# Performance work log

Measured on AMD Instinct MI355X. Metric: run time of the kernel, lower is better.

The kernel has to match this reference:

```python
import jax, jax.numpy as jnp
import numpy as np

N = 50000       # nodes
E = 800000      # edges
D_IN = 128      # input_dim
HID = 256       # hidden_dim
HEADS = 4
FH = HID // 4   # per-head out dim = 64
OUT = 8         # output_dim
NEG_SLOPE = 0.2 # GATConv leaky_relu slope


def setup_inputs() -> dict:
    key = jax.random.key(0)
    ks = jax.random.split(key, 16)
    def glorot(k, shape):
        fan_in, fan_out = shape[0], shape[-1]
        s = jnp.sqrt(6.0 / (fan_in + fan_out))
        return jax.random.uniform(k, shape, jnp.float32, -s, s)
    inp = {
        "x": jax.random.normal(ks[0], (N, D_IN), jnp.float32),
        "edge_index": jax.random.randint(ks[1], (2, E), 0, N, jnp.int64),
        # GCN layers
        "W1": glorot(ks[2], (D_IN, HID)), "b1": jnp.zeros((HID,), jnp.float32),
        "W2": glorot(ks[3], (HID, HID)), "b2": jnp.zeros((HID,), jnp.float32),
        "W3": glorot(ks[4], (HID, HID // 2)), "b3": jnp.zeros((HID // 2,), jnp.float32),
        # GAT layer: in = HID//2 = 128, out per head = FH, 4 heads concat -> HID
        "Wg": glorot(ks[5], (HID // 2, HEADS * FH)),
        "a_src": glorot(ks[6], (HEADS, FH)),
        "a_dst": glorot(ks[7], (HEADS, FH)),
        "bg": jnp.zeros((HEADS * FH,), jnp.float32),
        # classifier MLP: HID -> HID//2 -> HID//4 -> OUT
        "Wc1": glorot(ks[8], (HID, HID // 2)), "bc1": jnp.zeros((HID // 2,), jnp.float32),
        "Wc2": glorot(ks[9], (HID // 2, HID // 4)), "bc2": jnp.zeros((HID // 4,), jnp.float32),
        "Wc3": glorot(ks[10], (HID // 4, OUT)), "bc3": jnp.zeros((OUT,), jnp.float32),
    }
    return inp


def _with_self_loops(edge_index, n):
    loop = jnp.arange(n, dtype=edge_index.dtype)
    src = jnp.concatenate([edge_index[0], loop])
    dst = jnp.concatenate([edge_index[1], loop])
    return src, dst


def gcn_conv(x, W, b, src, dst, n):
    # PyG GCNConv: h = X W; out = D^{-1/2}(A+I)D^{-1/2} h + b (self loops in src/dst)
    h = x @ W
    deg = jax.ops.segment_sum(jnp.ones_like(dst, jnp.float32), dst, num_segments=n)
    dinv = jnp.where(deg > 0, jax.lax.rsqrt(deg), 0.0)
    norm = dinv[src] * dinv[dst]                      # [E+N]
    out = jax.ops.segment_sum(h[src] * norm[:, None], dst, num_segments=n)
    return out + b


def gat_conv(x, Wg, a_src, a_dst, bg, src, dst, n):
    # PyG GATConv (eval mode, no attn dropout), self loops included in src/dst
    h = (x @ Wg).reshape(n, HEADS, FH)                # [N,H,F]
    al_s = jnp.einsum('nhf,hf->nh', h, a_src)         # [N,H]
    al_d = jnp.einsum('nhf,hf->nh', h, a_dst)
    e = jax.nn.leaky_relu(al_s[src] + al_d[dst], NEG_SLOPE)  # [E+N,H]
    m = jax.ops.segment_max(e, dst, num_segments=n)   # per-dst stable softmax
    ex = jnp.exp(e - m[dst])
    den = jax.ops.segment_sum(ex, dst, num_segments=n)
    alpha = ex / den[dst]                             # [E+N,H]
    out = jax.ops.segment_sum(h[src] * alpha[:, :, None], dst, num_segments=n)
    return out.reshape(n, HEADS * FH) + bg


def reference(x, edge_index, W1, b1, W2, b2, W3, b3, Wg, a_src, a_dst, bg,
              Wc1, bc1, Wc2, bc2, Wc3, bc3):
    n = x.shape[0]
    src, dst = _with_self_loops(edge_index, n)
    h1 = jax.nn.relu(gcn_conv(x, W1, b1, src, dst, n))
    h2 = jax.nn.relu(gcn_conv(h1, W2, b2, src, dst, n)) + h1
    h3 = jax.nn.relu(gcn_conv(h2, W3, b3, src, dst, n))
    h_att = jax.nn.relu(gat_conv(h3, Wg, a_src, a_dst, bg, src, dst, n))
    h_pooled = jnp.mean(h_att, axis=0, keepdims=True)           # [1, HID]
    z = jax.nn.relu(h_pooled @ Wc1 + bc1)
    z = jax.nn.relu(z @ Wc2 + bc2)
    return z @ Wc3 + bc3                                        # [1, OUT]
```

## Files before the change

kernel.cpp:

```cpp
#include <hip/hip_runtime.h>
#include <hip/hip_bf16.h>

#define NNODES 50000
#define NEDGES 800000
#define EN 850000
#define SCAN_B 196

typedef __attribute__((ext_vector_type(8))) short bf16x8;
typedef __attribute__((ext_vector_type(4))) float f32x4;

__device__ __forceinline__ float bf2f(unsigned short u) {
    return __uint_as_float(((unsigned)u) << 16);
}
__device__ __forceinline__ float bflo(unsigned u) { return __uint_as_float(u << 16); }
__device__ __forceinline__ float bfhi(unsigned u) { return __uint_as_float(u & 0xffff0000u); }
__device__ __forceinline__ unsigned short f2bf(float x) {
    unsigned u = __float_as_uint(x);
    u += 0x7fffu + ((u >> 16) & 1u);
    return (unsigned short)(u >> 16);
}
__device__ __forceinline__ unsigned pack2bf(float a, float b) {
    return (unsigned)f2bf(a) | ((unsigned)f2bf(b) << 16);
}
__device__ __forceinline__ void acc8(float* acc, uint4 v, float wg) {
    acc[0] += bflo(v.x) * wg; acc[1] += bfhi(v.x) * wg;
    acc[2] += bflo(v.y) * wg; acc[3] += bfhi(v.y) * wg;
    acc[4] += bflo(v.z) * wg; acc[5] += bfhi(v.z) * wg;
    acc[6] += bflo(v.w) * wg; acc[7] += bfhi(v.w) * wg;
}

__device__ __forceinline__ void split_bf(float x, unsigned short& h, unsigned short& l) {
    unsigned u = __float_as_uint(x);
    h = (unsigned short)(u >> 16);
    float r = x - __uint_as_float(u & 0xffff0000u);
    l = (unsigned short)(__float_as_uint(r) >> 16);
}
__device__ __forceinline__ void do_split(const float* W, unsigned short* Wh, unsigned short* Wl,
                                         int i, int K, int N) {
    int n = i / K, k = i - n * K;
    unsigned short h, l;
    split_bf(W[(size_t)k * N + n], h, l);
    Wh[i] = h; Wl[i] = l;
}

__global__ __launch_bounds__(256) void prep_kernel(const int* __restrict__ ei, float* __restrict__ deg,
                                                   const float* __restrict__ x, unsigned short* __restrict__ xbf,
                                                   const float* __restrict__ W1, const float* __restrict__ W2,
                                                   const float* __restrict__ W3, const float* __restrict__ Wg,
                                                   unsigned short* __restrict__ W1th, unsigned short* __restrict__ W1tl,
                                                   unsigned short* __restrict__ W2th, unsigned short* __restrict__ W2tl,
                                                   unsigned short* __restrict__ W3th, unsigned short* __restrict__ W3tl,
                                                   unsigned short* __restrict__ Wgth, unsigned short* __restrict__ Wgtl) {
    int idx = blockIdx.x * 256 + threadIdx.x;
    atomicAdd(&deg[ei[NEDGES + idx]], 1.0f);
    {
        float4 a = *(const float4*)&x[(size_t)idx * 8];
        float4 b = *(const float4*)&x[(size_t)idx * 8 + 4];
        uint4 o;
        o.x = pack2bf(a.x, a.y); o.y = pack2bf(a.z, a.w);
        o.z = pack2bf(b.x, b.y); o.w = pack2bf(b.z, b.w);
        *(uint4*)&xbf[(size_t)idx * 8] = o;
    }
    if (idx < 32768)        do_split(W1, W1th, W1tl, idx, 128, 256);
    else if (idx < 98304)   do_split(W2, W2th, W2tl, idx - 32768, 256, 256);
    else if (idx < 131072)  do_split(W3, W3th, W3tl, idx - 98304, 256, 128);
    else if (idx < 163840)  do_split(Wg, Wgth, Wgtl, idx - 131072, 128, 256);
}

__global__ __launch_bounds__(256) void scan_part1(const float* __restrict__ deg, int* __restrict__ row,
                                                  int* __restrict__ bsum, float* __restrict__ dinv) {
    __shared__ int sdata[256];
    int t = threadIdx.x;
    int idx = blockIdx.x * 256 + t;
    float dg = idx < NNODES ? deg[idx] : 0.f;
    if (idx < NNODES) dinv[idx] = rsqrtf(dg + 1.0f);
    int v = idx < NNODES ? (int)dg + 1 : 0;
    sdata[t] = v;
    __syncthreads();
    for (int off = 1; off < 256; off <<= 1) {
        int tmp = t >= off ? sdata[t - off] : 0;
        __syncthreads();
        sdata[t] += tmp;
        __syncthreads();
    }
    if (idx < NNODES) row[idx] = sdata[t] - v;
    if (t == 255) bsum[blockIdx.x] = sdata[255];
}

__global__ __launch_bounds__(256) void scan_part2(int* __restrict__ bsum, int* __restrict__ bofs,
                                                  int* __restrict__ row) {
    __shared__ int sdata[256];
    int t = threadIdx.x;
    int v = t < SCAN_B ? bsum[t] : 0;
    sdata[t] = v;
    __syncthreads();
    for (int off = 1; off < 256; off <<= 1) {
        int tmp = t >= off ? sdata[t - off] : 0;
        __syncthreads();
        sdata[t] += tmp;
        __syncthreads();
    }
    if (t < SCAN_B) bofs[t] = sdata[t] - v;
    if (t == 0) row[NNODES] = EN;
}

__global__ __launch_bounds__(256) void scan_part3(int* __restrict__ row, const int* __restrict__ bofs) {
    int idx = blockIdx.x * 256 + threadIdx.x;
    if (idx < NNODES) row[idx] += bofs[blockIdx.x];
}

__global__ __launch_bounds__(256) void scatter_kernel(const int* __restrict__ ei, const int* __restrict__ row,
                                                      int* __restrict__ cursor, const float* __restrict__ dinv,
                                                      uint2* __restrict__ csr) {
    int e = blockIdx.x * blockDim.x + threadIdx.x;
    if (e >= EN) return;
    int s, d;
    if (e < NEDGES) { s = ei[e]; d = ei[NEDGES + e]; } else { s = e - NEDGES; d = s; }
    int pos = row[d] + atomicAdd(&cursor[d], 1);
    csr[pos] = make_uint2((unsigned)s, __float_as_uint(dinv[s] * dinv[d]));
}

template<int MODE>
__global__ __launch_bounds__(256) void gemm_bf(const unsigned short* __restrict__ A,
                                               const unsigned short* __restrict__ Wth,
                                               const unsigned short* __restrict__ Wtl,
                                               const float* __restrict__ bias,
                                               const float* __restrict__ asr, const float* __restrict__ ads,
                                               float* __restrict__ als, float* __restrict__ ald,
                                               unsigned short* __restrict__ C, int M, int K, int Nc) {
    __shared__ unsigned short As[128][40];
    __shared__ unsigned short Bh[128][40], Bl[128][40];
    int t = threadIdx.x;
    int row0 = blockIdx.x * 128, col0 = blockIdx.y * 128;
    int lane = t & 63, w = t >> 6;
    int mb = (w >> 1) * 64, nb = (w & 1) * 64;
    int lr = lane & 15, kg = (lane >> 4) * 8;

    f32x4 acc[4][4];
#pragma unroll
    for (int i = 0; i < 4; ++i)
#pragma unroll
        for (int j = 0; j < 4; ++j) acc[i][j] = (f32x4){0.f, 0.f, 0.f, 0.f};

    for (int k0 = 0; k0 < K; k0 += 32) {
#pragma unroll
        for (int it = 0; it < 2; ++it) {
            int q = it * 256 + t;
            int row = q >> 2, seg = (q & 3) * 8;
            int grow = row0 + row;
            uint4 v = make_uint4(0, 0, 0, 0);
            if (grow < M) v = *(const uint4*)&A[(size_t)grow * K + k0 + seg];
            *(uint4*)&As[row][seg] = v;
        }
#pragma unroll
        for (int it = 0; it < 2; ++it) {
            int o = it * 256 + t;
            int n = o >> 2, ko = (o & 3) * 8;
            size_t g = (size_t)(col0 + n) * K + k0 + ko;
            *(uint4*)&Bh[n][ko] = *(const uint4*)&Wth[g];
            *(uint4*)&Bl[n][ko] = *(const uint4*)&Wtl[g];
        }
        __syncthreads();

        bf16x8 a[4], bh[4], bl[4];
#pragma unroll
        for (int mf = 0; mf < 4; ++mf) a[mf] = *(const bf16x8*)&As[mb + mf * 16 + lr][kg];
#pragma unroll
        for (int nf = 0; nf < 4; ++nf) {
            bh[nf] = *(const bf16x8*)&Bh[nb + nf * 16 + lr][kg];
            bl[nf] = *(const bf16x8*)&Bl[nb + nf * 16 + lr][kg];
        }
#pragma unroll
        for (int mf = 0; mf < 4; ++mf)
#pragma unroll
            for (int nf = 0; nf < 4; ++nf) {
                acc[mf][nf] = __builtin_amdgcn_mfma_f32_16x16x32_bf16(a[mf], bh[nf], acc[mf][nf], 0, 0, 0);
                acc[mf][nf] = __builtin_amdgcn_mfma_f32_16x16x32_bf16(a[mf], bl[nf], acc[mf][nf], 0, 0, 0);
            }
        __syncthreads();
    }

    float s1[16], s2[16];
    if (MODE == 2) {
#pragma unroll
        for (int q = 0; q < 16; ++q) { s1[q] = 0.f; s2[q] = 0.f; }
    }

#pragma unroll
    for (int nf = 0; nf < 4; ++nf) {
        int col = col0 + nb + nf * 16 + lr;
        float bv = (MODE == 1) ? bias[col] : 0.f;
        float av = 0.f, dv = 0.f;
        if (MODE == 2) { av = asr[col]; dv = ads[col]; }
#pragma unroll
        for (int mf = 0; mf < 4; ++mf) {
#pragma unroll
            for (int r = 0; r < 4; ++r) {
                int row = row0 + mb + mf * 16 + (lane >> 4) * 4 + r;
                if (row < M) {
                    float v = acc[mf][nf][r];
                    if (MODE == 1) v = fmaxf(v + bv, 0.f);
                    C[(size_t)row * Nc + col] = f2bf(v);
                    if (MODE == 2) {
                        s1[mf * 4 + r] += v * av;
                        s2[mf * 4 + r] += v * dv;
                    }
                }
            }
        }
    }
    if (MODE == 2) {
        int head = (col0 + nb) >> 6;
#pragma unroll
        for (int q = 0; q < 16; ++q) {
#pragma unroll
            for (int off = 1; off < 16; off <<= 1) {
                s1[q] += __shfl_xor(s1[q], off);
                s2[q] += __shfl_xor(s2[q], off);
            }
        }
        if (lr == 0) {
#pragma unroll
            for (int mf = 0; mf < 4; ++mf) {
#pragma unroll
                for (int r = 0; r < 4; ++r) {
                    int row = row0 + mb + mf * 16 + (lane >> 4) * 4 + r;
                    if (row < M) {
                        als[row * 4 + head] = s1[mf * 4 + r];
                        ald[row * 4 + head] = s2[mf * 4 + r];
                    }
                }
            }
        }
    }
}

template<int NC, int MODE>
__global__ __launch_bounds__(256) void gcn_agg_bf(const unsigned short* __restrict__ h, const int* __restrict__ row,
                                                  const uint2* __restrict__ csr,
                                                  const float* __restrict__ b, const unsigned short* __restrict__ res,
                                                  unsigned short* __restrict__ out) {
    int wid = (int)((blockIdx.x * blockDim.x + threadIdx.x) >> 6);
    if (wid >= NNODES) return;
    int lane = threadIdx.x & 63;
    constexpr int LPE = NC / 8;
    constexpr int EPI = 64 / LPE;
    int sub = lane / LPE, li = lane % LPE;
    int col = li * 8;
    float acc[8];
#pragma unroll
    for (int i = 0; i < 8; ++i) acc[i] = 0.f;
    int j0 = row[wid], j1 = row[wid + 1];
    int j = j0 + sub;
    for (; j + 3 * EPI < j1; j += 4 * EPI) {
        uint2 c0 = csr[j], c1 = csr[j + EPI], c2 = csr[j + 2 * EPI], c3 = csr[j + 3 * EPI];
        uint4 v0 = *(const uint4*)&h[(size_t)c0.x * NC + col];
        uint4 v1 = *(const uint4*)&h[(size_t)c1.x * NC + col];
        uint4 v2 = *(const uint4*)&h[(size_t)c2.x * NC + col];
        uint4 v3 = *(const uint4*)&h[(size_t)c3.x * NC + col];
        acc8(acc, v0, __uint_as_float(c0.y));
        acc8(acc, v1, __uint_as_float(c1.y));
        acc8(acc, v2, __uint_as_float(c2.y));
        acc8(acc, v3, __uint_as_float(c3.y));
    }
    for (; j < j1; j += EPI) {
        uint2 c0 = csr[j];
        uint4 v0 = *(const uint4*)&h[(size_t)c0.x * NC + col];
        acc8(acc, v0, __uint_as_float(c0.y));
    }
#pragma unroll
    for (int i = 0; i < 8; ++i) {
        acc[i] += __shfl_xor(acc[i], 32);
        if constexpr (EPI == 4) acc[i] += __shfl_xor(acc[i], 16);
    }
    if (lane < LPE) {
        if constexpr (MODE >= 1) {
#pragma unroll
            for (int i = 0; i < 8; ++i) acc[i] = fmaxf(acc[i] + b[col + i], 0.f);
        }
        if constexpr (MODE == 2) {
            uint4 rv = *(const uint4*)&res[(size_t)wid * NC + col];
            acc8(acc, rv, 1.0f);
        }
        uint4 o;
        o.x = pack2bf(acc[0], acc[1]); o.y = pack2bf(acc[2], acc[3]);
        o.z = pack2bf(acc[4], acc[5]); o.w = pack2bf(acc[6], acc[7]);
        *(uint4*)&out[(size_t)wid * NC + col] = o;
    }
}

__device__ __forceinline__ float lrelu(float x) { return x < 0.f ? 0.2f * x : x; }

__global__ __launch_bounds__(256) void gat_csr(const unsigned short* __restrict__ hg, const int* __restrict__ row,
                                               const uint2* __restrict__ csr, const float* __restrict__ als,
                                               const float* __restrict__ ald, const float* __restrict__ bg,
                                               unsigned short* __restrict__ out) {
    __shared__ float alds[4][64][4];
    int wid = (int)((blockIdx.x * blockDim.x + threadIdx.x) >> 6);
    if (wid >= NNODES) return;
    int wv = threadIdx.x >> 6;
    int lane = threadIdx.x & 63;
    int j0 = row[wid], j1 = row[wid + 1];
    int deg = j1 - j0;
    float4 ad = *(const float4*)&ald[wid * 4];
    int sub = lane >> 5, li = lane & 31;
    int h = li >> 3;
    int col = li * 8;
    float acc[8];
#pragma unroll
    for (int i = 0; i < 8; ++i) acc[i] = 0.f;

    if (deg <= 64) {
        int sreg = 0;
        float e0 = -1e30f, e1 = -1e30f, e2 = -1e30f, e3 = -1e30f;
        if (lane < deg) {
            sreg = (int)csr[j0 + lane].x;
            float4 as4 = *(const float4*)&als[sreg * 4];
            e0 = lrelu(as4.x + ad.x); e1 = lrelu(as4.y + ad.y);
            e2 = lrelu(as4.z + ad.z); e3 = lrelu(as4.w + ad.w);
        }
        float m0 = e0, m1 = e1, m2 = e2, m3 = e3;
#pragma unroll
        for (int off = 32; off >= 1; off >>= 1) {
            m0 = fmaxf(m0, __shfl_xor(m0, off));
            m1 = fmaxf(m1, __shfl_xor(m1, off));
            m2 = fmaxf(m2, __shfl_xor(m2, off));
            m3 = fmaxf(m3, __shfl_xor(m3, off));
        }
        float x0 = __expf(e0 - m0), x1 = __expf(e1 - m1);
        float x2 = __expf(e2 - m2), x3 = __expf(e3 - m3);
        float d0 = x0, d1 = x1, d2 = x2, d3 = x3;
#pragma unroll
        for (int off = 32; off >= 1; off >>= 1) {
            d0 += __shfl_xor(d0, off);
            d1 += __shfl_xor(d1, off);
            d2 += __shfl_xor(d2, off);
            d3 += __shfl_xor(d3, off);
        }
        float i0 = 1.f / d0, i1 = 1.f / d1, i2 = 1.f / d2, i3 = 1.f / d3;
        *(float4*)&alds[wv][lane][0] = make_float4(x0 * i0, x1 * i1, x2 * i2, x3 * i3);
        int k = sub;
        for (; k + 6 < deg; k += 8) {
            int s0 = __shfl(sreg, k),     s1 = __shfl(sreg, k + 2);
            int s2 = __shfl(sreg, k + 4), s3 = __shfl(sreg, k + 6);
            float a0 = alds[wv][k][h],     a1 = alds[wv][k + 2][h];
            float a2 = alds[wv][k + 4][h], a3 = alds[wv][k + 6][h];
            uint4 v0 = *(const uint4*)&hg[(size_t)s0 * 256 + col];
            uint4 v1 = *(const uint4*)&hg[(size_t)s1 * 256 + col];
            uint4 v2 = *(const uint4*)&hg[(size_t)s2 * 256 + col];
            uint4 v3 = *(const uint4*)&hg[(size_t)s3 * 256 + col];
            acc8(acc, v0, a0); acc8(acc, v1, a1);
            acc8(acc, v2, a2); acc8(acc, v3, a3);
        }
        for (; k < deg; k += 2) {
            int s0 = __shfl(sreg, k);
            float a0 = alds[wv][k][h];
            uint4 v0 = *(const uint4*)&hg[(size_t)s0 * 256 + col];
            acc8(acc, v0, a0);
        }
    } else {
        float m0 = -1e30f, m1 = -1e30f, m2 = -1e30f, m3 = -1e30f;
        float d0 = 0.f, d1 = 0.f, d2 = 0.f, d3 = 0.f;
        for (int j = j0 + lane; j < j1; j += 64) {
            int s = (int)csr[j].x;
            float4 as4 = *(const float4*)&als[s * 4];
            m0 = fmaxf(m0, lrelu(as4.x + ad.x));
            m1 = fmaxf(m1, lrelu(as4.y + ad.y));
            m2 = fmaxf(m2, lrelu(as4.z + ad.z));
            m3 = fmaxf(m3, lrelu(as4.w + ad.w));
        }
#pragma unroll
        for (int off = 32; off >= 1; off >>= 1) {
            m0 = fmaxf(m0, __shfl_xor(m0, off));
            m1 = fmaxf(m1, __shfl_xor(m1, off));
            m2 = fmaxf(m2, __shfl_xor(m2, off));
            m3 = fmaxf(m3, __shfl_xor(m3, off));
        }
        for (int j = j0 + lane; j < j1; j += 64) {
            int s = (int)csr[j].x;
            float4 as4 = *(const float4*)&als[s * 4];
            d0 += __expf(lrelu(as4.x + ad.x) - m0);
            d1 += __expf(lrelu(as4.y + ad.y) - m1);
            d2 += __expf(lrelu(as4.z + ad.z) - m2);
            d3 += __expf(lrelu(as4.w + ad.w) - m3);
        }
#pragma unroll
        for (int off = 32; off >= 1; off >>= 1) {
            d0 += __shfl_xor(d0, off);
            d1 += __shfl_xor(d1, off);
            d2 += __shfl_xor(d2, off);
            d3 += __shfl_xor(d3, off);
        }
        float mh   = h == 0 ? m0 : h == 1 ? m1 : h == 2 ? m2 : m3;
        float invh = 1.f / (h == 0 ? d0 : h == 1 ? d1 : h == 2 ? d2 : d3);
        float adh  = h == 0 ? ad.x : h == 1 ? ad.y : h == 2 ? ad.z : ad.w;
        for (int j = j0 + sub; j < j1; j += 2) {
            uint2 c0 = csr[j];
            float a0 = __expf(lrelu(als[c0.x * 4 + h] + adh) - mh) * invh;
            uint4 v0 = *(const uint4*)&hg[(size_t)c0.x * 256 + col];
            acc8(acc, v0, a0);
        }
    }

#pragma unroll
    for (int i = 0; i < 8; ++i) acc[i] += __shfl_xor(acc[i], 32);
    if (lane < 32) {
        uint4 o;
        o.x = pack2bf(fmaxf(acc[0] + bg[col], 0.f),     fmaxf(acc[1] + bg[col + 1], 0.f));
        o.y = pack2bf(fmaxf(acc[2] + bg[col + 2], 0.f), fmaxf(acc[3] + bg[col + 3], 0.f));
        o.z = pack2bf(fmaxf(acc[4] + bg[col + 4], 0.f), fmaxf(acc[5] + bg[col + 5], 0.f));
        o.w = pack2bf(fmaxf(acc[6] + bg[col + 6], 0.f), fmaxf(acc[7] + bg[col + 7], 0.f));
        *(uint4*)&out[(size_t)wid * 256 + col] = o;
    }
}

__global__ __launch_bounds__(256) void pool_kernel(const unsigned short* __restrict__ hatt, float* __restrict__ ppart) {
    int col = threadIdx.x;
    int r0 = blockIdx.x * 256;
    int r1 = r0 + 256 < NNODES ? r0 + 256 : NNODES;
    float s = 0.f;
    for (int r = r0; r < r1; ++r) s += bf2f(hatt[(size_t)r * 256 + col]);
    ppart[blockIdx.x * 256 + col] = s;
}

__global__ __launch_bounds__(256) void mlp_kernel(const float* __restrict__ ppart,
                                                  const float* __restrict__ Wc1, const float* __restrict__ bc1,
                                                  const float* __restrict__ Wc2, const float* __restrict__ bc2,
                                                  const float* __restrict__ Wc3, const float* __restrict__ bc3,
                                                  float* __restrict__ out) {
    __shared__ float p[256], z1[128], z2[64];
    int t = threadIdx.x;
    float s0 = 0.f;
    for (int b = 0; b < SCAN_B; ++b) s0 += ppart[b * 256 + t];
    p[t] = s0 * (1.0f / NNODES);
    __syncthreads();
    if (t < 128) {
        float s = bc1[t];
        for (int k = 0; k < 256; ++k) s += p[k] * Wc1[k * 128 + t];
        z1[t] = fmaxf(s, 0.f);
    }
    __syncthreads();
    if (t < 64) {
        float s = bc2[t];
        for (int k = 0; k < 128; ++k) s += z1[k] * Wc2[k * 64 + t];
        z2[t] = fmaxf(s, 0.f);
    }
    __syncthreads();
    if (t < 8) {
        float s = bc3[t];
        for (int k = 0; k < 64; ++k) s += z2[k] * Wc3[k * 8 + t];
        out[t] = s;
    }
}

extern "C" void kernel_launch(void* const* d_in, const int* in_sizes, int n_in,
                              void* d_out, int out_size, void* d_ws, size_t ws_size,
                              hipStream_t stream) {
    const float* x   = (const float*)d_in[0];
    const int*   ei  = (const int*)d_in[1];
    const float* W1  = (const float*)d_in[2];  const float* b1  = (const float*)d_in[3];
    const float* W2  = (const float*)d_in[4];  const float* b2  = (const float*)d_in[5];
    const float* W3  = (const float*)d_in[6];  const float* b3  = (const float*)d_in[7];
    const float* Wg  = (const float*)d_in[8];
    const float* asr = (const float*)d_in[9];  const float* ads = (const float*)d_in[10];
    const float* bg  = (const float*)d_in[11];
    const float* Wc1 = (const float*)d_in[12]; const float* bc1 = (const float*)d_in[13];
    const float* Wc2 = (const float*)d_in[14]; const float* bc2 = (const float*)d_in[15];
    const float* Wc3 = (const float*)d_in[16]; const float* bc3 = (const float*)d_in[17];
    float* out = (float*)d_out;

    char* w = (char*)d_ws;
    float* deg    = (float*)w; w += (size_t)NNODES * 4;
    int*   cursor = (int*)w;   w += (size_t)NNODES * 4;
    float* dinv   = (float*)w; w += (size_t)NNODES * 4;
    int*   rowp   = (int*)w;   w += 200016;
    int*   bsum   = (int*)w;   w += 256 * 4;
    int*   bofs   = (int*)w;   w += 256 * 4;
    uint2* csr    = (uint2*)w; w += (size_t)EN * 8;
    float* als    = (float*)w; w += (size_t)NNODES * 4 * 4;
    float* ald    = (float*)w; w += (size_t)NNODES * 4 * 4;
    float* ppart  = (float*)w; w += (size_t)SCAN_B * 256 * 4;
    unsigned short* W1th = (unsigned short*)w; w += 128 * 256 * 2;
    unsigned short* W1tl = (unsigned short*)w; w += 128 * 256 * 2;
    unsigned short* W2th = (unsigned short*)w; w += 256 * 256 * 2;
    unsigned short* W2tl = (unsigned short*)w; w += 256 * 256 * 2;
    unsigned short* W3th = (unsigned short*)w; w += 256 * 128 * 2;
    unsigned short* W3tl = (unsigned short*)w; w += 256 * 128 * 2;
    unsigned short* Wgth = (unsigned short*)w; w += 128 * 256 * 2;
    unsigned short* Wgtl = (unsigned short*)w; w += 128 * 256 * 2;
    unsigned short* U1 = (unsigned short*)w; w += (size_t)NNODES * 256 * 2;
    unsigned short* U2 = (unsigned short*)w; w += (size_t)NNODES * 256 * 2;
    unsigned short* U3 = (unsigned short*)w; w += (size_t)NNODES * 256 * 2;
    unsigned short* U4 = (unsigned short*)w; w += (size_t)NNODES * 256 * 2;

    hipMemsetAsync(deg, 0, (size_t)NNODES * 8, stream);
    prep_kernel<<<3125, 256, 0, stream>>>(ei, deg, x, U1, W1, W2, W3, Wg,
                                          W1th, W1tl, W2th, W2tl, W3th, W3tl, Wgth, Wgtl);
    scan_part1<<<SCAN_B, 256, 0, stream>>>(deg, rowp, bsum, dinv);
    scan_part2<<<1, 256, 0, stream>>>(bsum, bofs, rowp);
    scan_part3<<<SCAN_B, 256, 0, stream>>>(rowp, bofs);
    scatter_kernel<<<(EN + 255) / 256, 256, 0, stream>>>(ei, rowp, cursor, dinv, csr);

    dim3 gA((NNODES + 127) / 128, 2);
    dim3 gB((NNODES + 127) / 128, 1);
    int aggBlocks = (NNODES * 64 + 255) / 256;

    gcn_agg_bf<128, 0><<<aggBlocks, 256, 0, stream>>>(U1, rowp, csr, nullptr, nullptr, U2);
    gemm_bf<1><<<gA, 256, 0, stream>>>(U2, W1th, W1tl, b1, nullptr, nullptr, nullptr, nullptr, U3, NNODES, 128, 256);

    gemm_bf<0><<<gA, 256, 0, stream>>>(U3, W2th, W2tl, nullptr, nullptr, nullptr, nullptr, nullptr, U1, NNODES, 256, 256);
    gcn_agg_bf<256, 2><<<aggBlocks, 256, 0, stream>>>(U1, rowp, csr, b2, U3, U2);

    gemm_bf<0><<<gB, 256, 0, stream>>>(U2, W3th, W3tl, nullptr, nullptr, nullptr, nullptr, nullptr, U4, NNODES, 256, 128);
    gcn_agg_bf<128, 1><<<aggBlocks, 256, 0, stream>>>(U4, rowp, csr, b3, nullptr, U1);

    gemm_bf<2><<<gA, 256, 0, stream>>>(U1, Wgth, Wgtl, nullptr, asr, ads, als, ald, U2, NNODES, 128, 256);
    gat_csr<<<aggBlocks, 256, 0, stream>>>(U2, rowp, csr, als, ald, bg, U3);

    pool_kernel<<<SCAN_B, 256, 0, stream>>>(U3, ppart);
    mlp_kernel<<<1, 256, 0, stream>>>(ppart, Wc1, bc1, Wc2, bc2, Wc3, bc3, out);
}
```

Baseline: 533.2 us.

## Fold attention logits into agg epilogue, fuse pooling into GAT, drop scan pass

Precomputes Wg·a_src and Wg·a_dst in the prep kernel so the per-node attention logits come from the third GCN aggregation epilogue, not from the GAT GEMM epilogue. The GAT kernel now writes per-block pooled partial sums instead of the full bf16 attention output, and a new reduce kernel feeds the MLP. The third scan pass is removed by adding the block offset wherever row pointers are read. This cuts one full-width activation write and read plus a launch, but adds a large partial buffer and changes the rounding of the logits, since they are now computed before the GEMM.

```diff
diff --git a/kernel.cpp b/kernel.cpp
--- a/kernel.cpp
+++ b/kernel.cpp
@@ -47,10 +47,12 @@
                                                    const float* __restrict__ x, unsigned short* __restrict__ xbf,
                                                    const float* __restrict__ W1, const float* __restrict__ W2,
                                                    const float* __restrict__ W3, const float* __restrict__ Wg,
+                                                   const float* __restrict__ asr, const float* __restrict__ ads,
                                                    unsigned short* __restrict__ W1th, unsigned short* __restrict__ W1tl,
                                                    unsigned short* __restrict__ W2th, unsigned short* __restrict__ W2tl,
                                                    unsigned short* __restrict__ W3th, unsigned short* __restrict__ W3tl,
-                                                   unsigned short* __restrict__ Wgth, unsigned short* __restrict__ Wgtl) {
+                                                   unsigned short* __restrict__ Wgth, unsigned short* __restrict__ Wgtl,
+                                                   float* __restrict__ asp, float* __restrict__ adp) {
     int idx = blockIdx.x * 256 + threadIdx.x;
     atomicAdd(&deg[ei[NEDGES + idx]], 1.0f);
     {
@@ -65,6 +67,18 @@
     else if (idx < 98304)   do_split(W2, W2th, W2tl, idx - 32768, 256, 256);
     else if (idx < 131072)  do_split(W3, W3th, W3tl, idx - 98304, 256, 128);
     else if (idx < 163840)  do_split(Wg, Wgth, Wgtl, idx - 131072, 128, 256);
+    else if (idx < 164864) {
+        int i0 = idx - 163840;
+        int which = i0 >> 9;
+        int h = (i0 >> 7) & 3;
+        int k = i0 & 127;
+        const float* av = (which ? ads : asr) + h * 64;
+        const float* wg = Wg + (size_t)k * 256 + h * 64;
+        float s = 0.f;
+#pragma unroll
+        for (int c = 0; c < 64; ++c) s += wg[c] * av[c];
+        (which ? adp : asp)[h * 128 + k] = s;
+    }
 }
 
 __global__ __launch_bounds__(256) void scan_part1(const float* __restrict__ deg, int* __restrict__ row,
@@ -101,22 +115,18 @@
         __syncthreads();
     }
     if (t < SCAN_B) bofs[t] = sdata[t] - v;
-    if (t == 0) row[NNODES] = EN;
-}
-
-__global__ __launch_bounds__(256) void scan_part3(int* __restrict__ row, const int* __restrict__ bofs) {
-    int idx = blockIdx.x * 256 + threadIdx.x;
-    if (idx < NNODES) row[idx] += bofs[blockIdx.x];
+    if (t == SCAN_B - 1) row[NNODES] = EN - (sdata[t] - v);
 }
 
 __global__ __launch_bounds__(256) void scatter_kernel(const int* __restrict__ ei, const int* __restrict__ row,
+                                                      const int* __restrict__ bofs,
                                                       int* __restrict__ cursor, const float* __restrict__ dinv,
                                                       uint2* __restrict__ csr) {
     int e = blockIdx.x * blockDim.x + threadIdx.x;
     if (e >= EN) return;
     int s, d;
     if (e < NEDGES) { s = ei[e]; d = ei[NEDGES + e]; } else { s = e - NEDGES; d = s; }
-    int pos = row[d] + atomicAdd(&cursor[d], 1);
+    int pos = row[d] + bofs[d >> 8] + atomicAdd(&cursor[d], 1);
     csr[pos] = make_uint2((unsigned)s, __float_as_uint(dinv[s] * dinv[d]));
 }
 
@@ -125,8 +135,6 @@
                                                const unsigned short* __restrict__ Wth,
                                                const unsigned short* __restrict__ Wtl,
                                                const float* __restrict__ bias,
-                                               const float* __restrict__ asr, const float* __restrict__ ads,
-                                               float* __restrict__ als, float* __restrict__ ald,
                                                unsigned short* __restrict__ C, int M, int K, int Nc) {
     __shared__ unsigned short As[128][40];
     __shared__ unsigned short Bh[128][40], Bl[128][40];
@@ -180,18 +188,10 @@
         __syncthreads();
     }
 
-    float s1[16], s2[16];
-    if (MODE == 2) {
-#pragma unroll
-        for (int q = 0; q < 16; ++q) { s1[q] = 0.f; s2[q] = 0.f; }
-    }
-
 #pragma unroll
     for (int nf = 0; nf < 4; ++nf) {
         int col = col0 + nb + nf * 16 + lr;
         float bv = (MODE == 1) ? bias[col] : 0.f;
-        float av = 0.f, dv = 0.f;
-        if (MODE == 2) { av = asr[col]; dv = ads[col]; }
 #pragma unroll
         for (int mf = 0; mf < 4; ++mf) {
 #pragma unroll
@@ -201,44 +201,18 @@
                     float v = acc[mf][nf][r];
                     if (MODE == 1) v = fmaxf(v + bv, 0.f);
                     C[(size_t)row * Nc + col] = f2bf(v);
-                    if (MODE == 2) {
-                        s1[mf * 4 + r] += v * av;
-                        s2[mf * 4 + r] += v * dv;
-                    }
                 }
             }
         }
     }
-    if (MODE == 2) {
-        int head = (col0 + nb) >> 6;
-#pragma unroll
-        for (int q = 0; q < 16; ++q) {
-#pragma unroll
-            for (int off = 1; off < 16; off <<= 1) {
-                s1[q] += __shfl_xor(s1[q], off);
-                s2[q] += __shfl_xor(s2[q], off);
-            }
-        }
-        if (lr == 0) {
-#pragma unroll
-            for (int mf = 0; mf < 4; ++mf) {
-#pragma unroll
-                for (int r = 0; r < 4; ++r) {
-                    int row = row0 + mb + mf * 16 + (lane >> 4) * 4 + r;
-                    if (row < M) {
-                        als[row * 4 + head] = s1[mf * 4 + r];
-                        ald[row * 4 + head] = s2[mf * 4 + r];
-                    }
-                }
-            }
-        }
-    }
 }
 
 template<int NC, int MODE>
 __global__ __launch_bounds__(256) void gcn_agg_bf(const unsigned short* __restrict__ h, const int* __restrict__ row,
-                                                  const uint2* __restrict__ csr,
+                                                  const int* __restrict__ bofs, const uint2* __restrict__ csr,
                                                   const float* __restrict__ b, const unsigned short* __restrict__ res,
+                                                  const float* __restrict__ asp, const float* __restrict__ adp,
+                                                  float* __restrict__ als, float* __restrict__ ald,
                                                   unsigned short* __restrict__ out) {
     int wid = (int)((blockIdx.x * blockDim.x + threadIdx.x) >> 6);
     if (wid >= NNODES) return;
@@ -250,7 +224,8 @@
     float acc[8];
 #pragma unroll
     for (int i = 0; i < 8; ++i) acc[i] = 0.f;
-    int j0 = row[wid], j1 = row[wid + 1];
+    int j0 = row[wid] + bofs[wid >> 8];
+    int j1 = row[wid + 1] + bofs[(wid + 1) >> 8];
     int j = j0 + sub;
     for (; j + 3 * EPI < j1; j += 4 * EPI) {
         uint2 c0 = csr[j], c1 = csr[j + EPI], c2 = csr[j + 2 * EPI], c3 = csr[j + 3 * EPI];
@@ -286,21 +261,47 @@
         o.x = pack2bf(acc[0], acc[1]); o.y = pack2bf(acc[2], acc[3]);
         o.z = pack2bf(acc[4], acc[5]); o.w = pack2bf(acc[6], acc[7]);
         *(uint4*)&out[(size_t)wid * NC + col] = o;
+        if constexpr (MODE == 3) {
+            float s1[4], s2[4];
+#pragma unroll
+            for (int hh = 0; hh < 4; ++hh) {
+                float t1 = 0.f, t2 = 0.f;
+#pragma unroll
+                for (int i = 0; i < 8; ++i) {
+                    t1 += acc[i] * asp[hh * 128 + col + i];
+                    t2 += acc[i] * adp[hh * 128 + col + i];
+                }
+                s1[hh] = t1; s2[hh] = t2;
+            }
+#pragma unroll
+            for (int off = 1; off <= 8; off <<= 1) {
+#pragma unroll
+                for (int hh = 0; hh < 4; ++hh) {
+                    s1[hh] += __shfl_xor(s1[hh], off);
+                    s2[hh] += __shfl_xor(s2[hh], off);
+                }
+            }
+            if (lane == 0) {
+                *(float4*)&als[wid * 4] = make_float4(s1[0], s1[1], s1[2], s1[3]);
+                *(float4*)&ald[wid * 4] = make_float4(s2[0], s2[1], s2[2], s2[3]);
+            }
+        }
     }
 }
 
 __device__ __forceinline__ float lrelu(float x) { return x < 0.f ? 0.2f * x : x; }
 
-__global__ __launch_bounds__(256) void gat_csr(const unsigned short* __restrict__ hg, const int* __restrict__ row,
-                                               const uint2* __restrict__ csr, const float* __restrict__ als,
-                                               const float* __restrict__ ald, const float* __restrict__ bg,
-                                               unsigned short* __restrict__ out) {
+__global__ __launch_bounds__(256) void gat_pool(const unsigned short* __restrict__ hg, const int* __restrict__ row,
+                                                const int* __restrict__ bofs, const uint2* __restrict__ csr,
+                                                const float* __restrict__ als, const float* __restrict__ ald,
+                                                const float* __restrict__ bg, float* __restrict__ ppart) {
     __shared__ float alds[4][64][4];
+    __shared__ float srows[4][256];
     int wid = (int)((blockIdx.x * blockDim.x + threadIdx.x) >> 6);
-    if (wid >= NNODES) return;
     int wv = threadIdx.x >> 6;
     int lane = threadIdx.x & 63;
-    int j0 = row[wid], j1 = row[wid + 1];
+    int j0 = row[wid] + bofs[wid >> 8];
+    int j1 = row[wid + 1] + bofs[(wid + 1) >> 8];
     int deg = j1 - j0;
     float4 ad = *(const float4*)&ald[wid * 4];
     int sub = lane >> 5, li = lane & 31;
@@ -337,8 +338,7 @@
             d2 += __shfl_xor(d2, off);
             d3 += __shfl_xor(d3, off);
         }
-        float i0 = 1.f / d0, i1 = 1.f / d1, i2 = 1.f / d2, i3 = 1.f / d3;
-        *(float4*)&alds[wv][lane][0] = make_float4(x0 * i0, x1 * i1, x2 * i2, x3 * i3);
+        *(float4*)&alds[wv][lane][0] = make_float4(x0 / d0, x1 / d1, x2 / d2, x3 / d3);
         int k = sub;
         for (; k + 6 < deg; k += 8) {
             int s0 = __shfl(sreg, k),     s1 = __shfl(sreg, k + 2);
@@ -405,25 +405,24 @@
 #pragma unroll
     for (int i = 0; i < 8; ++i) acc[i] += __shfl_xor(acc[i], 32);
     if (lane < 32) {
-        uint4 o;
-        o.x = pack2bf(fmaxf(acc[0] + bg[col], 0.f),     fmaxf(acc[1] + bg[col + 1], 0.f));
-        o.y = pack2bf(fmaxf(acc[2] + bg[col + 2], 0.f), fmaxf(acc[3] + bg[col + 3], 0.f));
-        o.z = pack2bf(fmaxf(acc[4] + bg[col + 4], 0.f), fmaxf(acc[5] + bg[col + 5], 0.f));
-        o.w = pack2bf(fmaxf(acc[6] + bg[col + 6], 0.f), fmaxf(acc[7] + bg[col + 7], 0.f));
-        *(uint4*)&out[(size_t)wid * 256 + col] = o;
-    }
-}
-
-__global__ __launch_bounds__(256) void pool_kernel(const unsigned short* __restrict__ hatt, float* __restrict__ ppart) {
-    int col = threadIdx.x;
-    int r0 = blockIdx.x * 256;
-    int r1 = r0 + 256 < NNODES ? r0 + 256 : NNODES;
+#pragma unroll
+        for (int i = 0; i < 8; ++i) srows[wv][col + i] = fmaxf(acc[i] + bg[col + i], 0.f);
+    }
+    __syncthreads();
+    int t = threadIdx.x;
+    ppart[(size_t)blockIdx.x * 256 + t] = srows[0][t] + srows[1][t] + srows[2][t] + srows[3][t];
+}
+
+__global__ __launch_bounds__(256) void reduce_kernel(const float* __restrict__ ppart, float* __restrict__ p2) {
+    int t = threadIdx.x;
+    int r0 = blockIdx.x * 64;
+    int r1 = r0 + 64 < 12500 ? r0 + 64 : 12500;
     float s = 0.f;
-    for (int r = r0; r < r1; ++r) s += bf2f(hatt[(size_t)r * 256 + col]);
-    ppart[blockIdx.x * 256 + col] = s;
-}
-
-__global__ __launch_bounds__(256) void mlp_kernel(const float* __restrict__ ppart,
+    for (int r = r0; r < r1; ++r) s += ppart[(size_t)r * 256 + t];
+    p2[blockIdx.x * 256 + t] = s;
+}
+
+__global__ __launch_bounds__(256) void mlp_kernel(const float* __restrict__ p2,
                                                   const float* __restrict__ Wc1, const float* __restrict__ bc1,
                                                   const float* __restrict__ Wc2, const float* __restrict__ bc2,
                                                   const float* __restrict__ Wc3, const float* __restrict__ bc3,
@@ -431,7 +430,7 @@
     __shared__ float p[256], z1[128], z2[64];
     int t = threadIdx.x;
     float s0 = 0.f;
-    for (int b = 0; b < SCAN_B; ++b) s0 += ppart[b * 256 + t];
+    for (int b = 0; b < SCAN_B; ++b) s0 += p2[b * 256 + t];
     p[t] = s0 * (1.0f / NNODES);
     __syncthreads();
     if (t < 128) {
@@ -479,7 +478,10 @@
     uint2* csr    = (uint2*)w; w += (size_t)EN * 8;
     float* als    = (float*)w; w += (size_t)NNODES * 4 * 4;
     float* ald    = (float*)w; w += (size_t)NNODES * 4 * 4;
-    float* ppart  = (float*)w; w += (size_t)SCAN_B * 256 * 4;
+    float* ppart  = (float*)w; w += (size_t)12500 * 256 * 4;
+    float* p2     = (float*)w; w += (size_t)SCAN_B * 256 * 4;
+    float* asp    = (float*)w; w += 4 * 128 * 4;
+    float* adp    = (float*)w; w += 4 * 128 * 4;
     unsigned short* W1th = (unsigned short*)w; w += 128 * 256 * 2;
     unsigned short* W1tl = (unsigned short*)w; w += 128 * 256 * 2;
     unsigned short* W2th = (unsigned short*)w; w += 256 * 256 * 2;
@@ -494,29 +496,31 @@
     unsigned short* U4 = (unsigned short*)w; w += (size_t)NNODES * 256 * 2;
 
     hipMemsetAsync(deg, 0, (size_t)NNODES * 8, stream);
-    prep_kernel<<<3125, 256, 0, stream>>>(ei, deg, x, U1, W1, W2, W3, Wg,
-                                          W1th, W1tl, W2th, W2tl, W3th, W3tl, Wgth, Wgtl);
+    prep_kernel<<<3125, 256, 0, stream>>>(ei, deg, x, U1, W1, W2, W3, Wg, asr, ads,
+                                          W1th, W1tl, W2th, W2tl, W3th, W3tl, Wgth, Wgtl, asp, adp);
     scan_part1<<<SCAN_B, 256, 0, stream>>>(deg, rowp, bsum, dinv);
     scan_part2<<<1, 256, 0, stream>>>(bsum, bofs, rowp);
-    scan_part3<<<SCAN_B, 256, 0, stream>>>(rowp, bofs);
-    scatter_kernel<<<(EN + 255) / 256, 256, 0, stream>>>(ei, rowp, cursor, dinv, csr);
+    scatter_kernel<<<(EN + 255) / 256, 256, 0, stream>>>(ei, rowp, bofs, cursor, dinv, csr);
 
     dim3 gA((NNODES + 127) / 128, 2);
     dim3 gB((NNODES + 127) / 128, 1);
     int aggBlocks = (NNODES * 64 + 255) / 256;
 
-    gcn_agg_bf<128, 0><<<aggBlocks, 256, 0, stream>>>(U1, rowp, csr, nullptr, nullptr, U2);
-    gemm_bf<1><<<gA, 256, 0, stream>>>(U2, W1th, W1tl, b1, nullptr, nullptr, nullptr, nullptr, U3, NNODES, 128, 256);
-
-    gemm_bf<0><<<gA, 256, 0, stream>>>(U3, W2th, W2tl, nullptr, nullptr, nullptr, nullptr, nullptr, U1, NNODES, 256, 256);
-    gcn_agg_bf<256, 2><<<aggBlocks, 256, 0, stream>>>(U1, rowp, csr, b2, U3, U2);
-
-    gemm_bf<0><<<gB, 256, 0, stream>>>(U2, W3th, W3tl, nullptr, nullptr, nullptr, nullptr, nullptr, U4, NNODES, 256, 128);
-    gcn_agg_bf<128, 1><<<aggBlocks, 256, 0, stream>>>(U4, rowp, csr, b3, nullptr, U1);
-
-    gemm_bf<2><<<gA, 256, 0, stream>>>(U1, Wgth, Wgtl, nullptr, asr, ads, als, ald, U2, NNODES, 128, 256);
-    gat_csr<<<aggBlocks, 256, 0, stream>>>(U2, rowp, csr, als, ald, bg, U3);
-
-    pool_kernel<<<SCAN_B, 256, 0, stream>>>(U3, ppart);
-    mlp_kernel<<<1, 256, 0, stream>>>(ppart, Wc1, bc1, Wc2, bc2, Wc3, bc3, out);
-}
+    gcn_agg_bf<128, 0><<<aggBlocks, 256, 0, stream>>>(U1, rowp, bofs, csr, nullptr, nullptr,
+                                                      nullptr, nullptr, nullptr, nullptr, U2);
+    gemm_bf<1><<<gA, 256, 0, stream>>>(U2, W1th, W1tl, b1, U3, NNODES, 128, 256);
+
+    gemm_bf<0><<<gA, 256, 0, stream>>>(U3, W2th, W2tl, nullptr, U1, NNODES, 256, 256);
+    gcn_agg_bf<256, 2><<<aggBlocks, 256, 0, stream>>>(U1, rowp, bofs, csr, b2, U3,
+                                                      nullptr, nullptr, nullptr, nullptr, U2);
+
+    gemm_bf<0><<<gB, 256, 0, stream>>>(U2, W3th, W3tl, nullptr, U4, NNODES, 256, 128);
+    gcn_agg_bf<128, 3><<<aggBlocks, 256, 0, stream>>>(U4, rowp, bofs, csr, b3, nullptr,
+                                                      asp, adp, als, ald, U1);
+
+    gemm_bf<0><<<gA, 256, 0, stream>>>(U1, Wgth, Wgtl, nullptr, U2, NNODES, 128, 256);
+    gat_pool<<<aggBlocks, 256, 0, stream>>>(U2, rowp, bofs, csr, als, ald, bg, ppart);
+
+    reduce_kernel<<<SCAN_B, 256, 0, stream>>>(ppart, p2);
+    mlp_kernel<<<1, 256, 0, stream>>>(p2, Wc1, bc1, Wc2, bc2, Wc3, bc3, out);
+}
```

After: 496.7 us (median of 2 runs). 6.8% less time.
